# Kernel tuning notes

Measured on AMD Instinct MI355X. Metric: run time of the kernel, lower is better.

## Reference

```python
import jax, jax.numpy as jnp
import numpy as np

N_NODES = 100000
N_EDGES = 3200000
F_IN, F_HID, F_OUT = 32, 32, 16


def spline_conv(x, edge_index, edge_attr, W, root, bias):
    """SplineConv, dim=1, kernel_size=2, degree=1, open spline, aggr='mean'.
    Basis weights over the 2 kernel slots are (1-u, u) for pseudo u in [0,1).
    W: [2, Fin, Fout], root: [Fin, Fout], bias: [Fout]."""
    src, dst = edge_index[0], edge_index[1]
    u = jnp.clip(edge_attr[:, 0:1], 0.0, 1.0)          # [E,1]
    x_src = x[src]                                      # [E,Fin] gather
    msg = (1.0 - u) * (x_src @ W[0]) + u * (x_src @ W[1])  # [E,Fout]
    agg = jax.ops.segment_sum(msg, dst, num_segments=x.shape[0])
    cnt = jax.ops.segment_sum(jnp.ones((msg.shape[0],), dtype=x.dtype), dst,
                              num_segments=x.shape[0])
    agg = agg / jnp.maximum(cnt, 1.0)[:, None]          # mean aggregation
    return agg + x @ root + bias


def setup_inputs() -> dict:
    key = jax.random.key(0)
    ks = jax.random.split(key, 9)
    x = jax.random.normal(ks[0], (N_NODES, F_IN), dtype=jnp.float32)
    edge_index = jax.random.randint(ks[1], (2, N_EDGES), 0, N_NODES, dtype=jnp.int64)
    edge_attr = jax.random.uniform(ks[2], (N_EDGES, 1), dtype=jnp.float32)
    s1 = 1.0 / np.sqrt(F_IN)
    s2 = 1.0 / np.sqrt(F_HID)
    W1 = jax.random.normal(ks[3], (2, F_IN, F_HID), dtype=jnp.float32) * s1
    root1 = jax.random.normal(ks[4], (F_IN, F_HID), dtype=jnp.float32) * s1
    b1 = jnp.zeros((F_HID,), dtype=jnp.float32)
    W2 = jax.random.normal(ks[5], (2, F_HID, F_OUT), dtype=jnp.float32) * s2
    root2 = jax.random.normal(ks[6], (F_HID, F_OUT), dtype=jnp.float32) * s2
    b2 = jnp.zeros((F_OUT,), dtype=jnp.float32)
    return {"x": x, "edge_index": edge_index, "edge_attr": edge_attr,
            "W1": W1, "root1": root1, "b1": b1,
            "W2": W2, "root2": root2, "b2": b2}


def reference(x, edge_index, edge_attr, W1, root1, b1, W2, root2, b2):
    # dropout is identity in eval mode
    h = jax.nn.relu(spline_conv(x, edge_index, edge_attr, W1, root1, b1))
    h = spline_conv(h, edge_index, edge_attr, W2, root2, b2)
    return jax.nn.log_softmax(h, axis=1)
```

## Files before the change

### kernel.cpp

```cpp
#include <hip/hip_runtime.h>
#include <math.h>

#define NN 100000
#define NE 3200000
#define BSH 6
#define BSZ 64
#define NBKT 1563
#define CAP 2560
#define STILE 8192
#define NTBS 391
#define NPB 1563
#define TST 68

#define FMA4(a, s, v) { (a).x += (s)*(v).x; (a).y += (s)*(v).y; (a).z += (s)*(v).z; (a).w += (s)*(v).w; }

typedef float v2f __attribute__((ext_vector_type(2)));

__device__ __forceinline__ unsigned fp8pack4(float a, float b, float c, float d) {
    int r = __builtin_amdgcn_cvt_pk_fp8_f32(a, b, 0, false);
    r = __builtin_amdgcn_cvt_pk_fp8_f32(c, d, r, true);
    return (unsigned)r;
}

#define LDE(pp, vv, idx) { int e_ = (idx); \
    if (e_ < cn) { pp = (unsigned)pks[cs + e_]; vv = x1[(size_t)(pp >> 15) * 8 + j]; } \
    else { pp = 0u; vv = 0u; } }
#define ACC(pp, vv) { float u_ = (float)((pp) & 511u) * (1.f / 511.f); \
    v2f lo_ = __builtin_amdgcn_cvt_pk_f32_fp8((vv), false); \
    v2f hi_ = __builtin_amdgcn_cvt_pk_f32_fp8((vv), true); \
    T0 += lo_.x; B0 += u_ * lo_.x;  T1 += lo_.y; B1 += u_ * lo_.y; \
    T2 += hi_.x; B2 += u_ * hi_.x;  T3 += hi_.y; B3 += u_ * hi_.y; }

__global__ __launch_bounds__(512) void sp_k(
    const int* __restrict__ ei, const float* __restrict__ ea,
    const float* __restrict__ x, const float* __restrict__ R, const float* __restrict__ b,
    int* __restrict__ bcur, int* __restrict__ pk,
    unsigned* __restrict__ xb, float* __restrict__ xr)
{
    __shared__ union {
        struct { int h[NBKT]; int base[NBKT]; } sc;
        struct { float Rs[1024]; float xs[64 * 33]; } pp;
    } sm;
    int t = threadIdx.x;

    if (blockIdx.x < NTBS) {
        for (int j = t; j < NBKT; j += 512) sm.sc.h[j] = 0;
        __syncthreads();
        int e0 = blockIdx.x * STILE + t;
        unsigned pck[16]; int bk[16], rk[16];
        #pragma unroll
        for (int i = 0; i < 16; i++) {
            int e = e0 + i * 512;
            bk[i] = -1;
            if (e < NE) {
                int s = ei[e];
                int d = ei[NE + e];
                float u = fminf(fmaxf(ea[e], 0.f), 1.f);
                unsigned uq = __float2uint_rn(u * 511.f);
                bk[i] = d >> BSH;
                pck[i] = ((unsigned)s << 15) | ((unsigned)(d & (BSZ - 1)) << 9) | uq;
                rk[i] = atomicAdd(&sm.sc.h[bk[i]], 1);
            }
        }
        __syncthreads();
        for (int j = t; j < NBKT; j += 512)
            sm.sc.base[j] = sm.sc.h[j] ? atomicAdd(&bcur[j], sm.sc.h[j]) : 0;
        __syncthreads();
        #pragma unroll
        for (int i = 0; i < 16; i++) {
            if (bk[i] >= 0) {
                int p = sm.sc.base[bk[i]] + rk[i];
                if (p < CAP) pk[(size_t)bk[i] * CAP + p] = (int)pck[i];
            }
        }
    } else {
        for (int i = t; i < 1024; i += 512) sm.pp.Rs[i] = R[i];
        int nb = (blockIdx.x - NTBS) * 64;
        for (int i = t; i < 2048; i += 512) {
            int n = nb + (i >> 5);
            sm.pp.xs[(i >> 5) * 33 + (i & 31)] = (n < NN) ? x[n * 32 + (i & 31)] : 0.f;
        }
        __syncthreads();
        int local = t >> 3, c = t & 7;
        int n = nb + local;
        float4 a2 = make_float4(0.f, 0.f, 0.f, 0.f);
        #pragma unroll
        for (int k = 0; k < 32; k++) {
            float xk = sm.pp.xs[local * 33 + k];
            float4 r = ((const float4*)sm.pp.Rs)[k * 8 + c];
            FMA4(a2, xk, r);
        }
        if (n < NN) {
            float4 bb = ((const float4*)b)[c];
            a2.x += bb.x; a2.y += bb.y; a2.z += bb.z; a2.w += bb.w;
            ((float4*)xr)[n * 8 + c] = a2;
            xb[n * 8 + c] = fp8pack4(sm.pp.xs[local * 33 + c * 4 + 0],
                                     sm.pp.xs[local * 33 + c * 4 + 1],
                                     sm.pp.xs[local * 33 + c * 4 + 2],
                                     sm.pp.xs[local * 33 + c * 4 + 3]);
        }
    }
}

__global__ __launch_bounds__(512, 6) void agg1_k(
    const int* __restrict__ bcur, const int* __restrict__ pk,
    const unsigned* __restrict__ xb, const float* __restrict__ W,
    const float* __restrict__ R2, const float* __restrict__ b2,
    const float* __restrict__ xr, unsigned* __restrict__ hb, float* __restrict__ hr)
{
    __shared__ float Wc[2048];
    __shared__ float R2s[512];
    __shared__ int ccnt[BSZ], coff[BSZ];
    __shared__ __align__(16) char smraw[BSZ * TST * 4];
    __shared__ float hs[BSZ * 33];
    int* pks = (int*)smraw;
    float* tb = (float*)smraw;

    int t = threadIdx.x;
    for (int i = t; i < 1024; i += 512) {
        float w0 = W[i];
        Wc[i] = w0;
        Wc[1024 + i] = W[1024 + i] - w0;
    }
    if (t < 512) R2s[t] = R2[t];
    if (t < BSZ) ccnt[t] = 0;
    __syncthreads();

    int bkt = blockIdx.x;
    int ne = bcur[bkt]; if (ne > CAP) ne = CAP;
    const int* sp = pk + (size_t)bkt * CAP;

    unsigned er[5]; int rk[5];
    #pragma unroll
    for (int i = 0; i < 5; i++) {
        int e = i * 512 + t;
        rk[i] = -1;
        if (e < ne) {
            er[i] = (unsigned)sp[e];
            rk[i] = atomicAdd(&ccnt[(er[i] >> 9) & (BSZ - 1)], 1);
        }
    }
    __syncthreads();
    if (t < BSZ) {
        int v = ccnt[t], sc = v;
        #pragma unroll
        for (int ofs = 1; ofs < 64; ofs <<= 1) {
            int nn = __shfl_up(sc, ofs);
            if (t >= ofs) sc += nn;
        }
        coff[t] = sc - v;
    }
    __syncthreads();
    #pragma unroll
    for (int i = 0; i < 5; i++)
        if (rk[i] >= 0) pks[coff[(er[i] >> 9) & (BSZ - 1)] + rk[i]] = (int)er[i];
    __syncthreads();

    int r = t >> 3, j = t & 7;
    int cs = coff[r], cn = ccnt[r];
    const unsigned* x1 = xb;
    float T0=0,T1=0,T2=0,T3=0,B0=0,B1=0,B2=0,B3=0;
    unsigned pa0, pa1, pa2, pa3, pb0, pb1, pb2, pb3;
    unsigned va0, va1, va2, va3, vb0, vb1, vb2, vb3;
    LDE(pa0, va0, 0) LDE(pa1, va1, 1) LDE(pa2, va2, 2) LDE(pa3, va3, 3)
    LDE(pb0, vb0, 4) LDE(pb1, vb1, 5) LDE(pb2, vb2, 6) LDE(pb3, vb3, 7)
    for (int k = 0; k < cn; k += 8) {
        ACC(pa0, va0) ACC(pa1, va1) ACC(pa2, va2) ACC(pa3, va3)
        LDE(pa0, va0, k + 8)  LDE(pa1, va1, k + 9)  LDE(pa2, va2, k + 10) LDE(pa3, va3, k + 11)
        ACC(pb0, vb0) ACC(pb1, vb1) ACC(pb2, vb2) ACC(pb3, vb3)
        LDE(pb0, vb0, k + 12) LDE(pb1, vb1, k + 13) LDE(pb2, vb2, k + 14) LDE(pb3, vb3, k + 15)
    }
    __syncthreads();

    ((float4*)(tb + r * TST + 4 * j))[0]      = make_float4(T0, T1, T2, T3);
    ((float4*)(tb + r * TST + 32 + 4 * j))[0] = make_float4(B0, B1, B2, B3);
    __syncthreads();

    {
        int row = t >> 3, cc = t & 7;
        int n = bkt * BSZ + row;
        float inv = 1.f / fmaxf((float)ccnt[row], 1.f);
        float4 acc = make_float4(0.f, 0.f, 0.f, 0.f);
        #pragma unroll
        for (int k = 0; k < 32; k++) {
            float sa = tb[row * TST + k];
            float4 w = ((const float4*)Wc)[k * 8 + cc];
            FMA4(acc, sa, w);
        }
        #pragma unroll
        for (int k = 0; k < 32; k++) {
            float sb = tb[row * TST + 32 + k];
            float4 w = ((const float4*)Wc)[(32 + k) * 8 + cc];
            FMA4(acc, sb, w);
        }
        float h0 = 0.f, h1 = 0.f, h2 = 0.f, h3 = 0.f;
        if (n < NN) {
            float4 rr = ((const float4*)xr)[n * 8 + cc];
            h0 = fmaxf(acc.x * inv + rr.x, 0.f);
            h1 = fmaxf(acc.y * inv + rr.y, 0.f);
            h2 = fmaxf(acc.z * inv + rr.z, 0.f);
            h3 = fmaxf(acc.w * inv + rr.w, 0.f);
            hb[n * 8 + cc] = fp8pack4(h0, h1, h2, h3);
        }
        hs[row * 33 + cc * 4 + 0] = h0;
        hs[row * 33 + cc * 4 + 1] = h1;
        hs[row * 33 + cc * 4 + 2] = h2;
        hs[row * 33 + cc * 4 + 3] = h3;
    }
    __syncthreads();

    #pragma unroll
    for (int p = 0; p < 2; p++) {
        int idx = p * 512 + t;
        int row = idx >> 4, f = idx & 15;
        int n = bkt * BSZ + row;
        if (n < NN) {
            float o = 0.f;
            #pragma unroll
            for (int k = 0; k < 32; k++) o += hs[row * 33 + k] * R2s[k * 16 + f];
            hr[n * 16 + f] = o + b2[f];
        }
    }
}

__global__ __launch_bounds__(512, 6) void agg2_k(
    const int* __restrict__ bcur, const int* __restrict__ pk,
    const unsigned* __restrict__ hb, const float* __restrict__ W,
    const float* __restrict__ hr, float* __restrict__ out)
{
    __shared__ float Wc[1024];
    __shared__ int ccnt[BSZ], coff[BSZ];
    __shared__ __align__(16) char smraw[BSZ * TST * 4];
    int* pks = (int*)smraw;
    float* tb = (float*)smraw;

    int t = threadIdx.x;
    if (t < 512) {
        float w0 = W[t];
        Wc[t] = w0;
        Wc[512 + t] = W[512 + t] - w0;
    }
    if (t < BSZ) ccnt[t] = 0;
    __syncthreads();

    int bkt = blockIdx.x;
    int ne = bcur[bkt]; if (ne > CAP) ne = CAP;
    const int* sp = pk + (size_t)bkt * CAP;

    unsigned er[5]; int rk[5];
    #pragma unroll
    for (int i = 0; i < 5; i++) {
        int e = i * 512 + t;
        rk[i] = -1;
        if (e < ne) {
            er[i] = (unsigned)sp[e];
            rk[i] = atomicAdd(&ccnt[(er[i] >> 9) & (BSZ - 1)], 1);
        }
    }
    __syncthreads();
    if (t < BSZ) {
        int v = ccnt[t], sc = v;
        #pragma unroll
        for (int ofs = 1; ofs < 64; ofs <<= 1) {
            int nn = __shfl_up(sc, ofs);
            if (t >= ofs) sc += nn;
        }
        coff[t] = sc - v;
    }
    __syncthreads();
    #pragma unroll
    for (int i = 0; i < 5; i++)
        if (rk[i] >= 0) pks[coff[(er[i] >> 9) & (BSZ - 1)] + rk[i]] = (int)er[i];
    __syncthreads();

    int r = t >> 3, j = t & 7;
    int cs = coff[r], cn = ccnt[r];
    const unsigned* x1 = hb;
    float T0=0,T1=0,T2=0,T3=0,B0=0,B1=0,B2=0,B3=0;
    unsigned pa0, pa1, pa2, pa3, pb0, pb1, pb2, pb3;
    unsigned va0, va1, va2, va3, vb0, vb1, vb2, vb3;
    LDE(pa0, va0, 0) LDE(pa1, va1, 1) LDE(pa2, va2, 2) LDE(pa3, va3, 3)
    LDE(pb0, vb0, 4) LDE(pb1, vb1, 5) LDE(pb2, vb2, 6) LDE(pb3, vb3, 7)
    for (int k = 0; k < cn; k += 8) {
        ACC(pa0, va0) ACC(pa1, va1) ACC(pa2, va2) ACC(pa3, va3)
        LDE(pa0, va0, k + 8)  LDE(pa1, va1, k + 9)  LDE(pa2, va2, k + 10) LDE(pa3, va3, k + 11)
        ACC(pb0, vb0) ACC(pb1, vb1) ACC(pb2, vb2) ACC(pb3, vb3)
        LDE(pb0, vb0, k + 12) LDE(pb1, vb1, k + 13) LDE(pb2, vb2, k + 14) LDE(pb3, vb3, k + 15)
    }
    __syncthreads();

    ((float4*)(tb + r * TST + 4 * j))[0]      = make_float4(T0, T1, T2, T3);
    ((float4*)(tb + r * TST + 32 + 4 * j))[0] = make_float4(B0, B1, B2, B3);
    __syncthreads();

    #pragma unroll
    for (int p = 0; p < 2; p++) {
        int row = p * 32 + (t >> 4), f = t & 15;
        int n = bkt * BSZ + row;
        float inv = 1.f / fmaxf((float)ccnt[row], 1.f);
        float o = 0.f;
        #pragma unroll
        for (int k = 0; k < 32; k++) o += tb[row * TST + k] * Wc[k * 16 + f];
        #pragma unroll
        for (int k = 0; k < 32; k++) o += tb[row * TST + 32 + k] * Wc[(32 + k) * 16 + f];
        if (n < NN) {
            o = o * inv + hr[n * 16 + f];
            float m = o;
            #pragma unroll
            for (int ofs = 8; ofs; ofs >>= 1) m = fmaxf(m, __shfl_xor(m, ofs, 16));
            float sm = expf(o - m);
            #pragma unroll
            for (int ofs = 8; ofs; ofs >>= 1) sm += __shfl_xor(sm, ofs, 16);
            out[n * 16 + f] = o - (m + logf(sm));
        }
    }
}

extern "C" void kernel_launch(void* const* d_in, const int* in_sizes, int n_in,
                              void* d_out, int out_size, void* d_ws, size_t ws_size,
                              hipStream_t stream) {
    const float* x     = (const float*)d_in[0];
    const int*   ei    = (const int*)d_in[1];
    const float* ea    = (const float*)d_in[2];
    const float* W1    = (const float*)d_in[3];
    const float* root1 = (const float*)d_in[4];
    const float* b1    = (const float*)d_in[5];
    const float* W2    = (const float*)d_in[6];
    const float* root2 = (const float*)d_in[7];
    const float* b2    = (const float*)d_in[8];
    float* out = (float*)d_out;

    int* ws = (int*)d_ws;
    int* bcur = ws;
    int* pk   = ws + 2048;
    size_t off = 2048 + (size_t)NBKT * CAP;
    unsigned* xb = (unsigned*)(ws + off);
    unsigned* hb = xb + (size_t)NN * 8;
    float* xr = (float*)(hb + (size_t)NN * 8);
    float* hr = xr + (size_t)NN * 32;

    hipMemsetAsync(bcur, 0, NBKT * sizeof(int), stream);

    sp_k   <<<NTBS + NPB, 512, 0, stream>>>(ei, ea, x, root1, b1, bcur, pk, xb, xr);
    agg1_k <<<NBKT, 512, 0, stream>>>(bcur, pk, xb, W1, root2, b2, xr, hb, hr);
    agg2_k <<<NBKT, 512, 0, stream>>>(bcur, pk, hb, W2, hr, out);
}
```

Baseline: 221.2 us.

## Replace global bucket atomics with per-tile local sort and offset table

The edge-binning kernel now counts destinations per tile in shared memory, scans them, sorts packed edges locally and writes each tile's edges contiguously, along with a per-tile 16-bit offset table. It replaces the global atomicAdd bucket counters and the memset. The aggregation kernels then scan the offsets across all 391 tiles and gather each bucket's edges from scattered segments into shared memory before processing. Scattered global writes become coalesced, at the cost of many small, poorly coalesced reads in both aggregation kernels and a larger shared-memory footprint.

```diff
diff --git a/kernel.cpp b/kernel.cpp
--- a/kernel.cpp
+++ b/kernel.cpp
@@ -11,6 +11,7 @@
 #define NTBS 391
 #define NPB 1563
 #define TST 68
+#define NOFF (NBKT + 1)
 
 #define FMA4(a, s, v) { (a).x += (s)*(v).x; (a).y += (s)*(v).y; (a).z += (s)*(v).z; (a).w += (s)*(v).w; }
 
@@ -34,45 +35,71 @@
 __global__ __launch_bounds__(512) void sp_k(
     const int* __restrict__ ei, const float* __restrict__ ea,
     const float* __restrict__ x, const float* __restrict__ R, const float* __restrict__ b,
-    int* __restrict__ bcur, int* __restrict__ pk,
+    int* __restrict__ pk, unsigned short* __restrict__ offs,
     unsigned* __restrict__ xb, float* __restrict__ xr)
 {
-    __shared__ union {
-        struct { int h[NBKT]; int base[NBKT]; } sc;
+    __shared__ __align__(16) union {
+        struct { int h[2048]; int staged[STILE]; } sc;
         struct { float Rs[1024]; float xs[64 * 33]; } pp;
     } sm;
     int t = threadIdx.x;
 
     if (blockIdx.x < NTBS) {
-        for (int j = t; j < NBKT; j += 512) sm.sc.h[j] = 0;
-        __syncthreads();
-        int e0 = blockIdx.x * STILE + t;
-        unsigned pck[16]; int bk[16], rk[16];
+        int* h = sm.sc.h;
+        for (int i = t; i < 2048; i += 512) h[i] = 0;
+        __syncthreads();
+        int e0 = blockIdx.x * STILE;
+        int cntblk = NE - e0; if (cntblk > STILE) cntblk = STILE;
+        int dreg[16];
         #pragma unroll
         for (int i = 0; i < 16; i++) {
-            int e = e0 + i * 512;
-            bk[i] = -1;
+            int e = e0 + i * 512 + t;
+            dreg[i] = -1;
             if (e < NE) {
-                int s = ei[e];
                 int d = ei[NE + e];
+                dreg[i] = d;
+                atomicAdd(&h[d >> BSH], 1);
+            }
+        }
+        __syncthreads();
+        int4 hc = ((const int4*)h)[t];
+        int s4 = hc.x + hc.y + hc.z + hc.w;
+        int lane = t & 63, wv = t >> 6;
+        int inc = s4;
+        #pragma unroll
+        for (int ofs = 1; ofs < 64; ofs <<= 1) {
+            int v = __shfl_up(inc, ofs);
+            if (lane >= ofs) inc += v;
+        }
+        int* wsum = sm.sc.staged;
+        if (lane == 63) wsum[wv] = inc;
+        __syncthreads();
+        int base = 0;
+        #pragma unroll
+        for (int i = 0; i < 8; i++) { int v = wsum[i]; if (i < wv) base += v; }
+        int ex = base + inc - s4;
+        ((int4*)h)[t] = make_int4(ex, ex + hc.x, ex + hc.x + hc.y, ex + hc.x + hc.y + hc.z);
+        __syncthreads();
+        for (int k = t; k < NOFF; k += 512)
+            offs[(size_t)blockIdx.x * NOFF + k] = (unsigned short)h[k];
+        __syncthreads();
+        #pragma unroll
+        for (int i = 0; i < 16; i++) {
+            int d = dreg[i];
+            if (d >= 0) {
+                int e = e0 + i * 512 + t;
+                int src = ei[e];
                 float u = fminf(fmaxf(ea[e], 0.f), 1.f);
                 unsigned uq = __float2uint_rn(u * 511.f);
-                bk[i] = d >> BSH;
-                pck[i] = ((unsigned)s << 15) | ((unsigned)(d & (BSZ - 1)) << 9) | uq;
-                rk[i] = atomicAdd(&sm.sc.h[bk[i]], 1);
+                unsigned pck = ((unsigned)src << 15) | ((unsigned)(d & (BSZ - 1)) << 9) | uq;
+                int pos = atomicAdd(&h[d >> BSH], 1);
+                sm.sc.staged[pos] = (int)pck;
             }
         }
         __syncthreads();
-        for (int j = t; j < NBKT; j += 512)
-            sm.sc.base[j] = sm.sc.h[j] ? atomicAdd(&bcur[j], sm.sc.h[j]) : 0;
-        __syncthreads();
-        #pragma unroll
-        for (int i = 0; i < 16; i++) {
-            if (bk[i] >= 0) {
-                int p = sm.sc.base[bk[i]] + rk[i];
-                if (p < CAP) pk[(size_t)bk[i] * CAP + p] = (int)pck[i];
-            }
-        }
+        int* seg = pk + (size_t)blockIdx.x * STILE;
+        for (int i = t; i * 4 < cntblk; i += 512)
+            ((int4*)seg)[i] = ((const int4*)sm.sc.staged)[i];
     } else {
         for (int i = t; i < 1024; i += 512) sm.pp.Rs[i] = R[i];
         int nb = (blockIdx.x - NTBS) * 64;
@@ -103,7 +130,7 @@
 }
 
 __global__ __launch_bounds__(512, 6) void agg1_k(
-    const int* __restrict__ bcur, const int* __restrict__ pk,
+    const int* __restrict__ pk, const unsigned short* __restrict__ offs,
     const unsigned* __restrict__ xb, const float* __restrict__ W,
     const float* __restrict__ R2, const float* __restrict__ b2,
     const float* __restrict__ xr, unsigned* __restrict__ hb, float* __restrict__ hr)
@@ -111,8 +138,9 @@
     __shared__ float Wc[2048];
     __shared__ float R2s[512];
     __shared__ int ccnt[BSZ], coff[BSZ];
+    __shared__ int wsum[8];
     __shared__ __align__(16) char smraw[BSZ * TST * 4];
-    __shared__ float hs[BSZ * 33];
+    __shared__ __align__(16) union { int staged[CAP]; float hs[BSZ * 33]; } su;
     int* pks = (int*)smraw;
     float* tb = (float*)smraw;
 
@@ -124,11 +152,38 @@
     }
     if (t < 512) R2s[t] = R2[t];
     if (t < BSZ) ccnt[t] = 0;
-    __syncthreads();
 
     int bkt = blockIdx.x;
-    int ne = bcur[bkt]; if (ne > CAP) ne = CAP;
-    const int* sp = pk + (size_t)bkt * CAP;
+    int cnt = 0, o0 = 0;
+    if (t < NTBS) {
+        size_t ob = (size_t)t * NOFF + bkt;
+        o0 = offs[ob];
+        cnt = (int)offs[ob + 1] - o0;
+    }
+    int lane = t & 63, wv = t >> 6;
+    int inc = cnt;
+    #pragma unroll
+    for (int ofs = 1; ofs < 64; ofs <<= 1) {
+        int v = __shfl_up(inc, ofs);
+        if (lane >= ofs) inc += v;
+    }
+    if (lane == 63) wsum[wv] = inc;
+    __syncthreads();
+    int base = 0, tot = 0;
+    #pragma unroll
+    for (int i = 0; i < 8; i++) { int v = wsum[i]; tot += v; if (i < wv) base += v; }
+    int dst = base + inc - cnt;
+    int ne = tot < CAP ? tot : CAP;
+    if (dst + cnt > CAP) { cnt = CAP - dst; if (cnt < 0) cnt = 0; }
+    const int* seg = pk + (size_t)t * STILE + o0;
+    int i2 = 0;
+    for (; i2 + 4 <= cnt; i2 += 4) {
+        int v0 = seg[i2], v1 = seg[i2 + 1], v2 = seg[i2 + 2], v3 = seg[i2 + 3];
+        su.staged[dst + i2] = v0; su.staged[dst + i2 + 1] = v1;
+        su.staged[dst + i2 + 2] = v2; su.staged[dst + i2 + 3] = v3;
+    }
+    for (; i2 < cnt; i2++) su.staged[dst + i2] = seg[i2];
+    __syncthreads();
 
     unsigned er[5]; int rk[5];
     #pragma unroll
@@ -136,7 +191,7 @@
         int e = i * 512 + t;
         rk[i] = -1;
         if (e < ne) {
-            er[i] = (unsigned)sp[e];
+            er[i] = (unsigned)su.staged[e];
             rk[i] = atomicAdd(&ccnt[(er[i] >> 9) & (BSZ - 1)], 1);
         }
     }
@@ -202,10 +257,10 @@
             h3 = fmaxf(acc.w * inv + rr.w, 0.f);
             hb[n * 8 + cc] = fp8pack4(h0, h1, h2, h3);
         }
-        hs[row * 33 + cc * 4 + 0] = h0;
-        hs[row * 33 + cc * 4 + 1] = h1;
-        hs[row * 33 + cc * 4 + 2] = h2;
-        hs[row * 33 + cc * 4 + 3] = h3;
+        su.hs[row * 33 + cc * 4 + 0] = h0;
+        su.hs[row * 33 + cc * 4 + 1] = h1;
+        su.hs[row * 33 + cc * 4 + 2] = h2;
+        su.hs[row * 33 + cc * 4 + 3] = h3;
     }
     __syncthreads();
 
@@ -217,20 +272,22 @@
         if (n < NN) {
             float o = 0.f;
             #pragma unroll
-            for (int k = 0; k < 32; k++) o += hs[row * 33 + k] * R2s[k * 16 + f];
+            for (int k = 0; k < 32; k++) o += su.hs[row * 33 + k] * R2s[k * 16 + f];
             hr[n * 16 + f] = o + b2[f];
         }
     }
 }
 
 __global__ __launch_bounds__(512, 6) void agg2_k(
-    const int* __restrict__ bcur, const int* __restrict__ pk,
+    const int* __restrict__ pk, const unsigned short* __restrict__ offs,
     const unsigned* __restrict__ hb, const float* __restrict__ W,
     const float* __restrict__ hr, float* __restrict__ out)
 {
     __shared__ float Wc[1024];
     __shared__ int ccnt[BSZ], coff[BSZ];
+    __shared__ int wsum[8];
     __shared__ __align__(16) char smraw[BSZ * TST * 4];
+    __shared__ __align__(16) int staged[CAP];
     int* pks = (int*)smraw;
     float* tb = (float*)smraw;
 
@@ -241,11 +298,38 @@
         Wc[512 + t] = W[512 + t] - w0;
     }
     if (t < BSZ) ccnt[t] = 0;
-    __syncthreads();
 
     int bkt = blockIdx.x;
-    int ne = bcur[bkt]; if (ne > CAP) ne = CAP;
-    const int* sp = pk + (size_t)bkt * CAP;
+    int cnt = 0, o0 = 0;
+    if (t < NTBS) {
+        size_t ob = (size_t)t * NOFF + bkt;
+        o0 = offs[ob];
+        cnt = (int)offs[ob + 1] - o0;
+    }
+    int lane = t & 63, wv = t >> 6;
+    int inc = cnt;
+    #pragma unroll
+    for (int ofs = 1; ofs < 64; ofs <<= 1) {
+        int v = __shfl_up(inc, ofs);
+        if (lane >= ofs) inc += v;
+    }
+    if (lane == 63) wsum[wv] = inc;
+    __syncthreads();
+    int base = 0, tot = 0;
+    #pragma unroll
+    for (int i = 0; i < 8; i++) { int v = wsum[i]; tot += v; if (i < wv) base += v; }
+    int dst = base + inc - cnt;
+    int ne = tot < CAP ? tot : CAP;
+    if (dst + cnt > CAP) { cnt = CAP - dst; if (cnt < 0) cnt = 0; }
+    const int* seg = pk + (size_t)t * STILE + o0;
+    int i2 = 0;
+    for (; i2 + 4 <= cnt; i2 += 4) {
+        int v0 = seg[i2], v1 = seg[i2 + 1], v2 = seg[i2 + 2], v3 = seg[i2 + 3];
+        staged[dst + i2] = v0; staged[dst + i2 + 1] = v1;
+        staged[dst + i2 + 2] = v2; staged[dst + i2 + 3] = v3;
+    }
+    for (; i2 < cnt; i2++) staged[dst + i2] = seg[i2];
+    __syncthreads();
 
     unsigned er[5]; int rk[5];
     #pragma unroll
@@ -253,7 +337,7 @@
         int e = i * 512 + t;
         rk[i] = -1;
         if (e < ne) {
-            er[i] = (unsigned)sp[e];
+            er[i] = (unsigned)staged[e];
             rk[i] = atomicAdd(&ccnt[(er[i] >> 9) & (BSZ - 1)], 1);
         }
     }
@@ -331,17 +415,15 @@
     float* out = (float*)d_out;
 
     int* ws = (int*)d_ws;
-    int* bcur = ws;
-    int* pk   = ws + 2048;
-    size_t off = 2048 + (size_t)NBKT * CAP;
-    unsigned* xb = (unsigned*)(ws + off);
+    int* pk = ws;
+    unsigned short* offs = (unsigned short*)(ws + NE);
+    size_t offw = (((size_t)NTBS * NOFF * 2 + 15) / 16) * 4;
+    unsigned* xb = (unsigned*)(ws + NE + offw);
     unsigned* hb = xb + (size_t)NN * 8;
     float* xr = (float*)(hb + (size_t)NN * 8);
     float* hr = xr + (size_t)NN * 32;
 
-    hipMemsetAsync(bcur, 0, NBKT * sizeof(int), stream);
-
-    sp_k   <<<NTBS + NPB, 512, 0, stream>>>(ei, ea, x, root1, b1, bcur, pk, xb, xr);
-    agg1_k <<<NBKT, 512, 0, stream>>>(bcur, pk, xb, W1, root2, b2, xr, hb, hr);
-    agg2_k <<<NBKT, 512, 0, stream>>>(bcur, pk, hb, W2, hr, out);
+    sp_k   <<<NTBS + NPB, 512, 0, stream>>>(ei, ea, x, root1, b1, pk, offs, xb, xr);
+    agg1_k <<<NBKT, 512, 0, stream>>>(pk, offs, xb, W1, root2, b2, xr, hb, hr);
+    agg2_k <<<NBKT, 512, 0, stream>>>(pk, offs, hb, W2, hr, out);
 }
```

Measured after the change: 237.0 us. 1.07x slower.

## Pad per-node edge lists to multiples of eight with zero sentinel records

Applied to the files above, without the earlier changes.

Each destination's edge segment in shared memory is rounded up to a multiple of eight and filled with sentinel records that point at a new zero row (node NN) in the fp8 feature tables. This lets the gather loop drop its per-element bounds branch. The accumulation also moves to packed two-wide float vectors, and the launch-bounds occupancy hint rises from 6 to 8 waves. Bucket capacity grows to hold the padding, at the cost of extra LDS and global workspace, and padded slots add some wasted gather loads.

```diff
diff --git a/kernel.cpp b/kernel.cpp
--- a/kernel.cpp
+++ b/kernel.cpp
@@ -6,11 +6,13 @@
 #define BSH 6
 #define BSZ 64
 #define NBKT 1563
-#define CAP 2560
+#define CAP 2816
 #define STILE 8192
 #define NTBS 391
 #define NPB 1563
 #define TST 68
+#define PADREC ((int)(100000u << 15))
+#define PKSFILL (CAP + 456)
 
 #define FMA4(a, s, v) { (a).x += (s)*(v).x; (a).y += (s)*(v).y; (a).z += (s)*(v).z; (a).w += (s)*(v).w; }
 
@@ -22,14 +24,31 @@
     return (unsigned)r;
 }
 
-#define LDE(pp, vv, idx) { int e_ = (idx); \
-    if (e_ < cn) { pp = (unsigned)pks[cs + e_]; vv = x1[(size_t)(pp >> 15) * 8 + j]; } \
-    else { pp = 0u; vv = 0u; } }
-#define ACC(pp, vv) { float u_ = (float)((pp) & 511u) * (1.f / 511.f); \
+#define LDEU(pp, vv, idx) { pp = (unsigned)pks[cs + (idx)]; vv = x1[(size_t)(pp >> 15) * 8 + j]; }
+#define ACCP(pp, vv) { float u_ = (float)((pp) & 511u) * (1.f / 511.f); \
+    v2f u2 = {u_, u_}; \
     v2f lo_ = __builtin_amdgcn_cvt_pk_f32_fp8((vv), false); \
     v2f hi_ = __builtin_amdgcn_cvt_pk_f32_fp8((vv), true); \
-    T0 += lo_.x; B0 += u_ * lo_.x;  T1 += lo_.y; B1 += u_ * lo_.y; \
-    T2 += hi_.x; B2 += u_ * hi_.x;  T3 += hi_.y; B3 += u_ * hi_.y; }
+    T01 += lo_; B01 += u2 * lo_; T23 += hi_; B23 += u2 * hi_; }
+
+#define WALK_BODY() \
+    int r = t >> 3, j = t & 7; \
+    int cs = coff[r], cn = ccnt[r], cnp = (cn + 7) & ~7; \
+    v2f T01 = {0.f,0.f}, T23 = {0.f,0.f}, B01 = {0.f,0.f}, B23 = {0.f,0.f}; \
+    unsigned pa0,pa1,pa2,pa3,pb0,pb1,pb2,pb3; \
+    unsigned va0,va1,va2,va3,vb0,vb1,vb2,vb3; \
+    LDEU(pa0,va0,0) LDEU(pa1,va1,1) LDEU(pa2,va2,2) LDEU(pa3,va3,3) \
+    LDEU(pb0,vb0,4) LDEU(pb1,vb1,5) LDEU(pb2,vb2,6) LDEU(pb3,vb3,7) \
+    for (int k = 0; k < cnp; k += 8) { \
+        ACCP(pa0,va0) ACCP(pa1,va1) ACCP(pa2,va2) ACCP(pa3,va3) \
+        LDEU(pa0,va0,k+8)  LDEU(pa1,va1,k+9)  LDEU(pa2,va2,k+10) LDEU(pa3,va3,k+11) \
+        ACCP(pb0,vb0) ACCP(pb1,vb1) ACCP(pb2,vb2) ACCP(pb3,vb3) \
+        LDEU(pb0,vb0,k+12) LDEU(pb1,vb1,k+13) LDEU(pb2,vb2,k+14) LDEU(pb3,vb3,k+15) \
+    } \
+    __syncthreads();                       \
+    ((float4*)(tb + r * TST + 4 * j))[0]      = make_float4(T01.x, T01.y, T23.x, T23.y); \
+    ((float4*)(tb + r * TST + 32 + 4 * j))[0] = make_float4(B01.x, B01.y, B23.x, B23.y); \
+    __syncthreads();
 
 __global__ __launch_bounds__(512) void sp_k(
     const int* __restrict__ ei, const float* __restrict__ ea,
@@ -44,7 +63,7 @@
     int t = threadIdx.x;
 
     if (blockIdx.x < NTBS) {
-        for (int j = t; j < NBKT; j += 512) sm.sc.h[j] = 0;
+        for (int jj = t; jj < NBKT; jj += 512) sm.sc.h[jj] = 0;
         __syncthreads();
         int e0 = blockIdx.x * STILE + t;
         unsigned pck[16]; int bk[16], rk[16];
@@ -63,8 +82,8 @@
             }
         }
         __syncthreads();
-        for (int j = t; j < NBKT; j += 512)
-            sm.sc.base[j] = sm.sc.h[j] ? atomicAdd(&bcur[j], sm.sc.h[j]) : 0;
+        for (int jj = t; jj < NBKT; jj += 512)
+            sm.sc.base[jj] = sm.sc.h[jj] ? atomicAdd(&bcur[jj], sm.sc.h[jj]) : 0;
         __syncthreads();
         #pragma unroll
         for (int i = 0; i < 16; i++) {
@@ -98,11 +117,13 @@
                                      sm.pp.xs[local * 33 + c * 4 + 1],
                                      sm.pp.xs[local * 33 + c * 4 + 2],
                                      sm.pp.xs[local * 33 + c * 4 + 3]);
-        }
-    }
-}
-
-__global__ __launch_bounds__(512, 6) void agg1_k(
+        } else if (n == NN) {
+            xb[n * 8 + c] = 0u;
+        }
+    }
+}
+
+__global__ __launch_bounds__(512, 8) void agg1_k(
     const int* __restrict__ bcur, const int* __restrict__ pk,
     const unsigned* __restrict__ xb, const float* __restrict__ W,
     const float* __restrict__ R2, const float* __restrict__ b2,
@@ -130,9 +151,9 @@
     int ne = bcur[bkt]; if (ne > CAP) ne = CAP;
     const int* sp = pk + (size_t)bkt * CAP;
 
-    unsigned er[5]; int rk[5];
-    #pragma unroll
-    for (int i = 0; i < 5; i++) {
+    unsigned er[6]; int rk[6];
+    #pragma unroll
+    for (int i = 0; i < 6; i++) {
         int e = i * 512 + t;
         rk[i] = -1;
         if (e < ne) {
@@ -142,39 +163,24 @@
     }
     __syncthreads();
     if (t < BSZ) {
-        int v = ccnt[t], sc = v;
+        int v = ccnt[t], vp = (v + 7) & ~7, sc = vp;
         #pragma unroll
         for (int ofs = 1; ofs < 64; ofs <<= 1) {
-            int nn = __shfl_up(sc, ofs);
-            if (t >= ofs) sc += nn;
-        }
-        coff[t] = sc - v;
-    }
-    __syncthreads();
-    #pragma unroll
-    for (int i = 0; i < 5; i++)
+            int nn2 = __shfl_up(sc, ofs);
+            if (t >= ofs) sc += nn2;
+        }
+        coff[t] = sc - vp;
+    } else {
+        for (int i = t - 64; i < PKSFILL; i += 448) pks[i] = PADREC;
+    }
+    __syncthreads();
+    #pragma unroll
+    for (int i = 0; i < 6; i++)
         if (rk[i] >= 0) pks[coff[(er[i] >> 9) & (BSZ - 1)] + rk[i]] = (int)er[i];
     __syncthreads();
 
-    int r = t >> 3, j = t & 7;
-    int cs = coff[r], cn = ccnt[r];
     const unsigned* x1 = xb;
-    float T0=0,T1=0,T2=0,T3=0,B0=0,B1=0,B2=0,B3=0;
-    unsigned pa0, pa1, pa2, pa3, pb0, pb1, pb2, pb3;
-    unsigned va0, va1, va2, va3, vb0, vb1, vb2, vb3;
-    LDE(pa0, va0, 0) LDE(pa1, va1, 1) LDE(pa2, va2, 2) LDE(pa3, va3, 3)
-    LDE(pb0, vb0, 4) LDE(pb1, vb1, 5) LDE(pb2, vb2, 6) LDE(pb3, vb3, 7)
-    for (int k = 0; k < cn; k += 8) {
-        ACC(pa0, va0) ACC(pa1, va1) ACC(pa2, va2) ACC(pa3, va3)
-        LDE(pa0, va0, k + 8)  LDE(pa1, va1, k + 9)  LDE(pa2, va2, k + 10) LDE(pa3, va3, k + 11)
-        ACC(pb0, vb0) ACC(pb1, vb1) ACC(pb2, vb2) ACC(pb3, vb3)
-        LDE(pb0, vb0, k + 12) LDE(pb1, vb1, k + 13) LDE(pb2, vb2, k + 14) LDE(pb3, vb3, k + 15)
-    }
-    __syncthreads();
-
-    ((float4*)(tb + r * TST + 4 * j))[0]      = make_float4(T0, T1, T2, T3);
-    ((float4*)(tb + r * TST + 32 + 4 * j))[0] = make_float4(B0, B1, B2, B3);
-    __syncthreads();
+    WALK_BODY()
 
     {
         int row = t >> 3, cc = t & 7;
@@ -201,6 +207,8 @@
             h2 = fmaxf(acc.z * inv + rr.z, 0.f);
             h3 = fmaxf(acc.w * inv + rr.w, 0.f);
             hb[n * 8 + cc] = fp8pack4(h0, h1, h2, h3);
+        } else if (n == NN) {
+            hb[n * 8 + cc] = 0u;
         }
         hs[row * 33 + cc * 4 + 0] = h0;
         hs[row * 33 + cc * 4 + 1] = h1;
@@ -223,7 +231,7 @@
     }
 }
 
-__global__ __launch_bounds__(512, 6) void agg2_k(
+__global__ __launch_bounds__(512, 8) void agg2_k(
     const int* __restrict__ bcur, const int* __restrict__ pk,
     const unsigned* __restrict__ hb, const float* __restrict__ W,
     const float* __restrict__ hr, float* __restrict__ out)
@@ -247,9 +255,9 @@
     int ne = bcur[bkt]; if (ne > CAP) ne = CAP;
     const int* sp = pk + (size_t)bkt * CAP;
 
-    unsigned er[5]; int rk[5];
-    #pragma unroll
-    for (int i = 0; i < 5; i++) {
+    unsigned er[6]; int rk[6];
+    #pragma unroll
+    for (int i = 0; i < 6; i++) {
         int e = i * 512 + t;
         rk[i] = -1;
         if (e < ne) {
@@ -259,39 +267,24 @@
     }
     __syncthreads();
     if (t < BSZ) {
-        int v = ccnt[t], sc = v;
+        int v = ccnt[t], vp = (v + 7) & ~7, sc = vp;
         #pragma unroll
         for (int ofs = 1; ofs < 64; ofs <<= 1) {
-            int nn = __shfl_up(sc, ofs);
-            if (t >= ofs) sc += nn;
-        }
-        coff[t] = sc - v;
-    }
-    __syncthreads();
-    #pragma unroll
-    for (int i = 0; i < 5; i++)
+            int nn2 = __shfl_up(sc, ofs);
+            if (t >= ofs) sc += nn2;
+        }
+        coff[t] = sc - vp;
+    } else {
+        for (int i = t - 64; i < PKSFILL; i += 448) pks[i] = PADREC;
+    }
+    __syncthreads();
+    #pragma unroll
+    for (int i = 0; i < 6; i++)
         if (rk[i] >= 0) pks[coff[(er[i] >> 9) & (BSZ - 1)] + rk[i]] = (int)er[i];
     __syncthreads();
 
-    int r = t >> 3, j = t & 7;
-    int cs = coff[r], cn = ccnt[r];
     const unsigned* x1 = hb;
-    float T0=0,T1=0,T2=0,T3=0,B0=0,B1=0,B2=0,B3=0;
-    unsigned pa0, pa1, pa2, pa3, pb0, pb1, pb2, pb3;
-    unsigned va0, va1, va2, va3, vb0, vb1, vb2, vb3;
-    LDE(pa0, va0, 0) LDE(pa1, va1, 1) LDE(pa2, va2, 2) LDE(pa3, va3, 3)
-    LDE(pb0, vb0, 4) LDE(pb1, vb1, 5) LDE(pb2, vb2, 6) LDE(pb3, vb3, 7)
-    for (int k = 0; k < cn; k += 8) {
-        ACC(pa0, va0) ACC(pa1, va1) ACC(pa2, va2) ACC(pa3, va3)
-        LDE(pa0, va0, k + 8)  LDE(pa1, va1, k + 9)  LDE(pa2, va2, k + 10) LDE(pa3, va3, k + 11)
-        ACC(pb0, vb0) ACC(pb1, vb1) ACC(pb2, vb2) ACC(pb3, vb3)
-        LDE(pb0, vb0, k + 12) LDE(pb1, vb1, k + 13) LDE(pb2, vb2, k + 14) LDE(pb3, vb3, k + 15)
-    }
-    __syncthreads();
-
-    ((float4*)(tb + r * TST + 4 * j))[0]      = make_float4(T0, T1, T2, T3);
-    ((float4*)(tb + r * TST + 32 + 4 * j))[0] = make_float4(B0, B1, B2, B3);
-    __syncthreads();
+    WALK_BODY()
 
     #pragma unroll
     for (int p = 0; p < 2; p++) {
@@ -332,12 +325,17 @@
 
     int* ws = (int*)d_ws;
     int* bcur = ws;
-    int* pk   = ws + 2048;
-    size_t off = 2048 + (size_t)NBKT * CAP;
-    unsigned* xb = (unsigned*)(ws + off);
-    unsigned* hb = xb + (size_t)NN * 8;
-    float* xr = (float*)(hb + (size_t)NN * 8);
-    float* hr = xr + (size_t)NN * 32;
+    size_t o_pk = 2048;
+    size_t o_xb = o_pk + (size_t)NBKT * CAP;
+    size_t o_hb = o_xb + (size_t)(NN + 1) * 8;
+    size_t o_xr = o_hb + (size_t)(NN + 1) * 8;
+    size_t o_hr = o_xr + (size_t)NN * 32;
+
+    int* pk = ws + o_pk;
+    unsigned* xb = (unsigned*)(ws + o_xb);
+    unsigned* hb = (unsigned*)(ws + o_hb);
+    float* xr = (float*)(ws + o_xr);
+    float* hr = (float*)(ws + o_hr);
 
     hipMemsetAsync(bcur, 0, NBKT * sizeof(int), stream);
 
```

After: 215.6 us, median of 2. -2.5%, faster.
